# Optimization experiments

Hardware: AMD Instinct MI355X
Metric: run time of the kernel (lower is better)

The kernel has to match this reference:

```python
import jax, jax.numpy as jnp
import numpy as np

B, S, D, H = 2, 2048, 2048, 16
HD = D // H          # 128, even for RoPE
GS = 0.1             # governance_strength
ROPE_BASE = 10000.0


def _rope_cos_sin(seq_len, dtype):
    # inv_freq over pairs of dims: [HD/2]
    inv_freq = 1.0 / (ROPE_BASE ** (jnp.arange(0, HD, 2, dtype=jnp.float32) / HD))
    t = jnp.arange(seq_len, dtype=jnp.float32)
    freqs = jnp.outer(t, inv_freq)          # [S, HD/2]
    return jnp.cos(freqs).astype(dtype), jnp.sin(freqs).astype(dtype)


def _apply_rope(x, cos, sin):
    # x: [B,H,S,HD]; cos/sin: [S,HD/2] -> broadcast over batch/heads
    x1, x2 = jnp.split(x, 2, axis=-1)
    c = cos[None, None, :, :]
    s = sin[None, None, :, :]
    return jnp.concatenate([x1 * c - x2 * s, x2 * c + x1 * s], axis=-1)


def setup_inputs() -> dict:
    key = jax.random.key(0)
    ks = jax.random.split(key, 8)
    sc = 1.0 / np.sqrt(D)
    return {
        "x": jax.random.normal(ks[0], (B, S, D), jnp.float32),
        "Wq": jax.random.normal(ks[1], (D, D), jnp.float32) * sc,
        "Wk": jax.random.normal(ks[2], (D, D), jnp.float32) * sc,
        "Wv": jax.random.normal(ks[3], (D, D), jnp.float32) * sc,
        "Wo": jax.random.normal(ks[4], (D, D), jnp.float32) * sc,
        "bo": jnp.zeros((D,), jnp.float32),
        "policy_mask": jax.random.uniform(ks[5], (1, H, S, S), jnp.float32),
        "memory_weights": jax.random.uniform(ks[6], (B, 1, 1, S), jnp.float32),
    }


def reference(x, Wq, Wk, Wv, Wo, bo, policy_mask, memory_weights):
    dtype = x.dtype
    scale = HD ** -0.5

    def heads(t):
        return t.reshape(B, S, H, HD).transpose(0, 2, 1, 3)  # [B,H,S,HD]

    q = heads(x @ Wq)
    k = heads(x @ Wk)
    v = heads(x @ Wv)

    cos, sin = _rope_cos_sin(S, dtype)
    q = _apply_rope(q, cos, sin)
    k = _apply_rope(k, cos, sin)

    scores = jnp.einsum("bhqd,bhkd->bhqk", q, k) * scale  # [B,H,S,S]

    # governance bias: policy term + memory-aware log term
    bias = policy_mask * GS + jnp.log1p(memory_weights * GS + 1e-8)
    scores = scores + bias

    # causal mask (no KV cache: kv_len == q_len)
    causal = jnp.tril(jnp.ones((S, S), bool))[None, None]
    scores = jnp.where(causal, scores, jnp.asarray(-1e9, dtype))

    attn = jax.nn.softmax(scores, axis=-1)
    out = jnp.einsum("bhqk,bhkd->bhqd", attn, v)          # [B,H,S,HD]
    out = out.transpose(0, 2, 1, 3).reshape(B, S, D)
    return out @ Wo + bo
```

## Files before the change

### kernel.cpp

```cpp
#include <hip/hip_runtime.h>
#include <hip/hip_bf16.h>
#include <math.h>

#define B_ 2
#define S_ 2048
#define D_ 2048
#define H_ 16
#define HD_ 128
#define NT_ (B_*S_)
#define GS_ 0.1f

typedef _Float16 half8 __attribute__((__vector_size__(16)));
typedef _Float16 half4v __attribute__((__vector_size__(8)));
typedef _Float16 half2v __attribute__((__vector_size__(4)));
typedef float f32x4 __attribute__((__vector_size__(16)));
typedef float f32x16 __attribute__((__vector_size__(64)));

__device__ __forceinline__ void gload_lds16(const void* g, void* s) {
  __builtin_amdgcn_global_load_lds(
      (const __attribute__((address_space(1))) unsigned int*)g,
      (__attribute__((address_space(3))) unsigned int*)s, 16, 0, 0);
}


__global__ void cvt_f32_to_f16(const float* __restrict__ in, _Float16* __restrict__ out, int n4) {
  int i = blockIdx.x * blockDim.x + threadIdx.x;
  if (i >= n4) return;
  float4 v = ((const float4*)in)[i];
  half4v o = { (_Float16)v.x, (_Float16)v.y, (_Float16)v.z, (_Float16)v.w };
  ((half4v*)out)[i] = o;
}

__global__ void transpose_to_f16(const float* __restrict__ in, _Float16* __restrict__ out, int R, int C) {
  __shared__ float t[32][33];
  int c0 = blockIdx.x*32, r0 = blockIdx.y*32;
  int tx = threadIdx.x, ty = threadIdx.y;
#pragma unroll
  for (int j = 0; j < 32; j += 8)
    t[ty+j][tx] = in[(size_t)(r0+ty+j)*C + c0+tx];
  __syncthreads();
#pragma unroll
  for (int j = 0; j < 32; j += 8)
    out[(size_t)(c0+ty+j)*R + r0+tx] = (_Float16)t[tx][ty+j];
}

__global__ void prep_tables(const float* __restrict__ mw, float* __restrict__ cost,
                            float* __restrict__ sint, float* __restrict__ lmw) {
  int t = blockIdx.x*256 + threadIdx.x;
  if (t < S_*64) {
    int s = t >> 6, d = t & 63;
    float inv = (float)pow(10000.0, -(double)(2*d)/(double)HD_);
    float f = (float)s * inv;
    cost[t] = cosf(f);
    sint[t] = sinf(f);
  }
  if (t < B_*S_) lmw[t] = log1pf(mw[t]*GS_ + 1e-8f);
}


template<bool F32OUT>
__global__ __launch_bounds__(256) void gemm_f16(
    const _Float16* __restrict__ A, const _Float16* __restrict__ Bt,
    void* __restrict__ Cout, const float* __restrict__ bias,
    int M, int N, int K)
{
  __shared__ __align__(16) _Float16 As[128*64];
  __shared__ __align__(16) _Float16 Bs[128*64];
  int n0 = blockIdx.x*128, m0 = blockIdx.y*128;
  int tid = threadIdx.x;
  int w = tid >> 6, l = tid & 63;
  int lhi = l >> 4, llo = l & 15;
  int wr = w >> 1, wc = w & 1;
  const f32x4 fz = {0.f,0.f,0.f,0.f};
  f32x4 acc[4][4];
#pragma unroll
  for (int i = 0; i < 4; ++i)
#pragma unroll
    for (int j = 0; j < 4; ++j) acc[i][j] = fz;

  for (int kt = 0; kt < K; kt += 64) {
#pragma unroll
    for (int i = 0; i < 4; ++i) {
      int sid = i*256 + tid;
      int row = sid >> 3;
      int c   = (sid & 7) ^ (row & 7);
      gload_lds16(A  + (size_t)(m0+row)*K + kt + c*8, (char*)As + (size_t)(i*256 + w*64)*16);
      gload_lds16(Bt + (size_t)(n0+row)*K + kt + c*8, (char*)Bs + (size_t)(i*256 + w*64)*16);
    }
    __syncthreads();
#pragma unroll
    for (int kk = 0; kk < 2; ++kk) {
      half8 a[4], b[4];
#pragma unroll
      for (int mi = 0; mi < 4; ++mi) {
        int row = wr*64 + mi*16 + llo;
        int ch = (kk*4 + lhi) ^ (row & 7);
        a[mi] = *(const half8*)((const char*)As + row*128 + ch*16);
      }
#pragma unroll
      for (int ni = 0; ni < 4; ++ni) {
        int row = wc*64 + ni*16 + llo;
        int ch = (kk*4 + lhi) ^ (row & 7);
        b[ni] = *(const half8*)((const char*)Bs + row*128 + ch*16);
      }
#pragma unroll
      for (int mi = 0; mi < 4; ++mi)
#pragma unroll
        for (int ni = 0; ni < 4; ++ni)
          acc[mi][ni] = __builtin_amdgcn_mfma_f32_16x16x32_f16(a[mi], b[ni], acc[mi][ni], 0, 0, 0);
    }
    __syncthreads();
  }
#pragma unroll
  for (int mi = 0; mi < 4; ++mi)
#pragma unroll
    for (int ni = 0; ni < 4; ++ni)
#pragma unroll
      for (int r = 0; r < 4; ++r) {
        int row = m0 + wr*64 + mi*16 + lhi*4 + r;
        int col = n0 + wc*64 + ni*16 + llo;
        if constexpr (F32OUT)
          ((float*)Cout)[(size_t)row*N + col] = acc[mi][ni][r] + bias[col];
        else
          ((_Float16*)Cout)[(size_t)row*N + col] = (_Float16)acc[mi][ni][r];
      }
}

__global__ void rope_qk(const _Float16* __restrict__ qkv, const float* __restrict__ cost,
                        const float* __restrict__ sint, _Float16* __restrict__ Qr,
                        _Float16* __restrict__ Kr) {
  int token = blockIdx.x;
  int b = token >> 11, s = token & (S_-1);
  int t = threadIdx.x;
  int isk = t >> 7, u = t & 127;
  int hh = u >> 3, dd0 = (u & 7)*8;
  const _Float16* src = qkv + (size_t)token*(3*D_) + (size_t)isk*D_ + hh*128;
  half8 a  = *(const half8*)(src + dd0);
  half8 bb = *(const half8*)(src + 64 + dd0);
  half8 lo, hi;
#pragma unroll
  for (int j = 0; j < 8; ++j) {
    float c  = cost[s*64 + dd0 + j];
    float sn = sint[s*64 + dd0 + j];
    float x1 = (float)a[j], x2 = (float)bb[j];
    lo[j] = (_Float16)(x1*c - x2*sn);
    hi[j] = (_Float16)(x2*c + x1*sn);
  }
  _Float16* dst = (isk ? Kr : Qr) + ((size_t)(b*H_ + hh)*S_ + s)*HD_;
  *(half8*)(dst + dd0) = lo;
  *(half8*)(dst + 64 + dd0) = hi;
}

__global__ void v_transpose(const _Float16* __restrict__ qkv, _Float16* __restrict__ Vt) {
  __shared__ _Float16 tile[64][33];
  int st = blockIdx.x*64;
  int dt = blockIdx.y*32;
  int bh = blockIdx.z;
  int b = bh >> 4, h = bh & 15;
  int t = threadIdx.x;
  int s = t >> 2, dc = (t & 3)*8;
  half8 v = *(const half8*)(qkv + (size_t)(b*S_ + st + s)*(3*D_) + 2*D_ + h*128 + dt + dc);
#pragma unroll
  for (int j = 0; j < 8; ++j) tile[s][dc+j] = v[j];
  __syncthreads();
  int d = t >> 3, sc = (t & 7)*8;
  half8 o;
#pragma unroll
  for (int j = 0; j < 8; ++j) o[j] = tile[sc+j][d];
  *(half8*)(Vt + ((size_t)bh*HD_ + dt + d)*S_ + st + sc) = o;
}

__global__ __launch_bounds__(256) void attn_kernel(
    const _Float16* __restrict__ Qr, const _Float16* __restrict__ Kr,
    const _Float16* __restrict__ Vt, const float* __restrict__ policy,
    const float* __restrict__ lmw, _Float16* __restrict__ Ob)
{
  __shared__ __align__(16) char SMEM[32768];
  char* Kl = SMEM;
  char* Vl = SMEM + 16384;
  int bx = blockIdx.x;
  int qb = (S_/128) - 1 - (bx / (B_*H_));
  int rem = bx % (B_*H_);
  int h = rem >> 1;
  int b = rem & 1;
  int bh = b*H_ + h;
  const _Float16* Qb = Qr + (size_t)bh*S_*HD_;
  const _Float16* Kb = Kr + (size_t)bh*S_*HD_;
  const _Float16* Vb = Vt + (size_t)bh*HD_*S_;
  const float* pol = policy + (size_t)h*S_*S_;
  const float* lmb = lmw + b*S_;
  int tid = threadIdx.x;
  int w = tid >> 6, l = tid & 63;
  int l31 = l & 31, lh = l >> 5;
  int q0 = qb*128 + w*32;
  int gq = q0 + l31;

  const float scale = 0.08838834764831845f;
  half8 qf[8];
#pragma unroll
  for (int ds = 0; ds < 8; ++ds) {
    half8 qv = *(const half8*)(Qb + (size_t)gq*HD_ + ds*16 + lh*8);
#pragma unroll
    for (int e = 0; e < 8; ++e) qv[e] = (_Float16)((float)qv[e] * scale);
    qf[ds] = qv;
  }

  f32x16 oacc[4];
#pragma unroll
  for (int i = 0; i < 4; ++i)
#pragma unroll
    for (int r = 0; r < 16; ++r) oacc[i][r] = 0.f;
  float m_ = -INFINITY, l_ = 0.f;

  int nt = qb*2 + 2;
  for (int t = 0; t < nt; ++t) {
    int kv0 = t*64;
#pragma unroll
    for (int i = 0; i < 4; ++i) {
      int sid = i*256 + tid;
      int krow = sid >> 4;
      int ck = (sid & 15) ^ (krow & 15);
      gload_lds16(Kb + (size_t)(kv0+krow)*HD_ + ck*8, Kl + (size_t)(i*256 + w*64)*16);
      int co = (sid & 15) ^ (krow & 15);
      int dv = krow*2 + (co >> 3);
      gload_lds16(Vb + (size_t)dv*S_ + kv0 + (co & 7)*8, Vl + (size_t)(i*256 + w*64)*16);
    }
    __syncthreads();

    f32x16 sacc[2];
#pragma unroll
    for (int kh = 0; kh < 2; ++kh)
#pragma unroll
      for (int r = 0; r < 16; ++r) sacc[kh][r] = 0.f;
    __builtin_amdgcn_s_setprio(1);
#pragma unroll
    for (int kh = 0; kh < 2; ++kh) {
      const char* kbase = Kl + (kh*32 + l31)*256;
      int sw = l & 15;
#pragma unroll
      for (int ds = 0; ds < 8; ++ds) {
        half8 kf = *(const half8*)(kbase + (((ds*2 + lh) ^ sw) << 4));
        sacc[kh] = __builtin_amdgcn_mfma_f32_32x32x16_f16(kf, qf[ds], sacc[kh], 0, 0, 0);
      }
    }
    __builtin_amdgcn_s_setprio(0);

    bool domask = (kv0 + 63 > q0);
#pragma unroll
    for (int kh = 0; kh < 2; ++kh) {
      float po[16], lm_[16];
#pragma unroll
      for (int g = 0; g < 4; ++g) {
        int gk0 = kv0 + kh*32 + g*8 + lh*4;
        float4 p4 = *(const float4*)(pol + (size_t)gq*S_ + gk0);
        float4 l4 = *(const float4*)(lmb + gk0);
        po[g*4+0]=p4.x; po[g*4+1]=p4.y; po[g*4+2]=p4.z; po[g*4+3]=p4.w;
        lm_[g*4+0]=l4.x; lm_[g*4+1]=l4.y; lm_[g*4+2]=l4.z; lm_[g*4+3]=l4.w;
      }
#pragma unroll
      for (int r = 0; r < 16; ++r) {
        float v = fmaf(po[r], GS_, sacc[kh][r] + lm_[r]);
        int gk = kv0 + kh*32 + (r&3) + 8*(r>>2) + 4*lh;
        if (domask && gk > gq) v = -1e9f;
        sacc[kh][r] = v;
      }
    }

    float mx = -INFINITY;
#pragma unroll
    for (int kh = 0; kh < 2; ++kh)
#pragma unroll
      for (int r = 0; r < 16; ++r) mx = fmaxf(mx, sacc[kh][r]);
    mx = fmaxf(mx, __shfl_xor(mx, 32));
    bool skip = __all(mx - m_ <= 8.0f);
    if (!skip) {
      float mnew = fmaxf(m_, mx);
      float fct = __expf(m_ - mnew);
      m_ = mnew;
      l_ *= fct;
#pragma unroll
      for (int i = 0; i < 4; ++i)
#pragma unroll
        for (int r = 0; r < 16; ++r) oacc[i][r] *= fct;
    }
    float rsum = 0.f;
#pragma unroll
    for (int kh = 0; kh < 2; ++kh)
#pragma unroll
      for (int r = 0; r < 16; ++r) {
        float pp = __expf(sacc[kh][r] - m_);
        sacc[kh][r] = pp;
        rsum += pp;
      }
    rsum += __shfl_xor(rsum, 32);
    l_ += rsum;

    half8 pfrag[4];
#pragma unroll
    for (int s = 0; s < 4; ++s) {
      int kh = s >> 1, rb = (s & 1)*8;
      unsigned A0 = __builtin_bit_cast(unsigned, __builtin_amdgcn_cvt_pkrtz(sacc[kh][rb+0], sacc[kh][rb+1]));
      unsigned A1 = __builtin_bit_cast(unsigned, __builtin_amdgcn_cvt_pkrtz(sacc[kh][rb+2], sacc[kh][rb+3]));
      unsigned B0 = __builtin_bit_cast(unsigned, __builtin_amdgcn_cvt_pkrtz(sacc[kh][rb+4], sacc[kh][rb+5]));
      unsigned B1 = __builtin_bit_cast(unsigned, __builtin_amdgcn_cvt_pkrtz(sacc[kh][rb+6], sacc[kh][rb+7]));
      unsigned sA0 = (unsigned)__shfl_xor((int)A0, 32);
      unsigned sA1 = (unsigned)__shfl_xor((int)A1, 32);
      unsigned sB0 = (unsigned)__shfl_xor((int)B0, 32);
      unsigned sB1 = (unsigned)__shfl_xor((int)B1, 32);
      uint4 uu;
      uu.x = lh ? sB0 : A0;
      uu.y = lh ? sB1 : A1;
      uu.z = lh ? B0  : sA0;
      uu.w = lh ? B1  : sA1;
      pfrag[s] = __builtin_bit_cast(half8, uu);
    }

    __builtin_amdgcn_s_setprio(1);
#pragma unroll
    for (int dt = 0; dt < 4; ++dt) {
      int d = dt*32 + l31;
      const char* vbase = Vl + (d >> 1)*256;
      int swv = l31 >> 1;
      int cbase = (d & 1) << 3;
#pragma unroll
      for (int s = 0; s < 4; ++s) {
        half8 vf = *(const half8*)(vbase + (((cbase + s*2 + lh) ^ swv) << 4));
        oacc[dt] = __builtin_amdgcn_mfma_f32_32x32x16_f16(vf, pfrag[s], oacc[dt], 0, 0, 0);
      }
    }
    __builtin_amdgcn_s_setprio(0);
    __syncthreads();
  }

  float inv = 1.f / l_;
  int q = w*32 + l31;
#pragma unroll
  for (int dt = 0; dt < 4; ++dt)
#pragma unroll
    for (int rq = 0; rq < 4; ++rq) {
      half4v o4;
#pragma unroll
      for (int j = 0; j < 4; ++j) o4[j] = (_Float16)(oacc[dt][rq*4+j] * inv);
      int off = q*256 + ((dt*64 + rq*16 + lh*8) ^ ((q & 15) << 4));
      *(half4v*)(SMEM + off) = o4;
    }
  __syncthreads();
  int qr = tid >> 1, hf = tid & 1;
  size_t gbase = ((size_t)(b*S_ + qb*128 + qr))*D_ + h*128 + hf*64;
#pragma unroll
  for (int j = 0; j < 8; ++j) {
    int c = hf*8 + j;
    half8 vv = *(const half8*)(SMEM + qr*256 + ((c ^ (qr & 15)) << 4));
    *(half8*)(Ob + gbase + j*8) = vv;
  }
}


extern "C" void kernel_launch(void* const* d_in, const int* in_sizes, int n_in,
                              void* d_out, int out_size, void* d_ws, size_t ws_size,
                              hipStream_t stream) {
  const float* x   = (const float*)d_in[0];
  const float* Wq  = (const float*)d_in[1];
  const float* Wk  = (const float*)d_in[2];
  const float* Wv  = (const float*)d_in[3];
  const float* Wo  = (const float*)d_in[4];
  const float* bo  = (const float*)d_in[5];
  const float* pol = (const float*)d_in[6];
  const float* mw  = (const float*)d_in[7];
  float* out = (float*)d_out;

  char* p = (char*)d_ws;
  auto take = [&](size_t bytes) { char* r = p; p += (bytes + 255) & ~(size_t)255; return r; };
  _Float16* xb   = (_Float16*)take((size_t)NT_*D_*2);
  _Float16* Wt   = (_Float16*)take((size_t)3*D_*D_*2);
  _Float16* Wot  = (_Float16*)take((size_t)D_*D_*2);
  _Float16* qkv  = (_Float16*)take((size_t)NT_*3*D_*2);
  _Float16* Qr   = (_Float16*)take((size_t)B_*H_*S_*HD_*2);
  _Float16* Kr   = (_Float16*)take((size_t)B_*H_*S_*HD_*2);
  _Float16* Vtb  = (_Float16*)take((size_t)B_*H_*S_*HD_*2);
  _Float16* Ob   = (_Float16*)take((size_t)NT_*D_*2);
  float* cost = (float*)take((size_t)S_*64*4);
  float* sint = (float*)take((size_t)S_*64*4);
  float* lmwb = (float*)take((size_t)B_*S_*4);

  cvt_f32_to_f16<<<(NT_*D_/4 + 255)/256, 256, 0, stream>>>(x, xb, NT_*D_/4);
  transpose_to_f16<<<dim3(64,64), dim3(32,8), 0, stream>>>(Wq, Wt,                    D_, D_);
  transpose_to_f16<<<dim3(64,64), dim3(32,8), 0, stream>>>(Wk, Wt +   (size_t)D_*D_,  D_, D_);
  transpose_to_f16<<<dim3(64,64), dim3(32,8), 0, stream>>>(Wv, Wt + 2*(size_t)D_*D_,  D_, D_);
  transpose_to_f16<<<dim3(64,64), dim3(32,8), 0, stream>>>(Wo, Wot, D_, D_);
  prep_tables<<<512, 256, 0, stream>>>(mw, cost, sint, lmwb);

  gemm_f16<false><<<dim3(3*D_/128, NT_/128), 256, 0, stream>>>(xb, Wt, qkv, nullptr, NT_, 3*D_, D_);
  rope_qk<<<NT_, 256, 0, stream>>>(qkv, cost, sint, Qr, Kr);
  v_transpose<<<dim3(S_/64, HD_/32, B_*H_), 256, 0, stream>>>(qkv, Vtb);
  attn_kernel<<<B_*H_*(S_/128), 256, 0, stream>>>(Qr, Kr, Vtb, pol, lmwb, Ob);
  gemm_f16<true><<<dim3(D_/128, NT_/128), 256, 0, stream>>>(Ob, Wot, out, bo, NT_, D_, D_);
}
```

Measured before the change: 368.6 us.

## Double-buffer K/V tiles in LDS and coalesce policy-bias loads via LDS

Allocates two LDS buffers for the K/V tiles and prefetches the next tile with global_load_lds while the current tile's QK and PV MFMAs run, using explicit vmcnt waits and raw s_barrier instead of __syncthreads. The policy mask and log-memory bias are now loaded row-coalesced per wave, folded into fp16 in a per-wave LDS scratch, then read back in MFMA accumulator layout. The aim is to hide global latency and avoid strided policy loads. In exchange, LDS use grows to 80KB, which may cut occupancy, and the bias is rounded to fp16, a small precision loss.

```diff
diff --git a/kernel.cpp b/kernel.cpp
--- a/kernel.cpp
+++ b/kernel.cpp
@@ -15,6 +15,8 @@
 typedef _Float16 half2v __attribute__((__vector_size__(4)));
 typedef float f32x4 __attribute__((__vector_size__(16)));
 typedef float f32x16 __attribute__((__vector_size__(64)));
+
+#define VMCNT(n) asm volatile("s_waitcnt vmcnt(" #n ")" ::: "memory")
 
 __device__ __forceinline__ void gload_lds16(const void* g, void* s) {
   __builtin_amdgcn_global_load_lds(
@@ -175,9 +177,7 @@
     const _Float16* __restrict__ Vt, const float* __restrict__ policy,
     const float* __restrict__ lmw, _Float16* __restrict__ Ob)
 {
-  __shared__ __align__(16) char SMEM[32768];
-  char* Kl = SMEM;
-  char* Vl = SMEM + 16384;
+  __shared__ __align__(16) char SMEM[81920];
   int bx = blockIdx.x;
   int qb = (S_/128) - 1 - (bx / (B_*H_));
   int rem = bx % (B_*H_);
@@ -192,40 +192,65 @@
   int tid = threadIdx.x;
   int w = tid >> 6, l = tid & 63;
   int l31 = l & 31, lh = l >> 5;
+  int r8 = l >> 3, c8 = l & 7;
   int q0 = qb*128 + w*32;
   int gq = q0 + l31;
-
-  const float scale = 0.08838834764831845f;
-  half8 qf[8];
-#pragma unroll
-  for (int ds = 0; ds < 8; ++ds) {
-    half8 qv = *(const half8*)(Qb + (size_t)gq*HD_ + ds*16 + lh*8);
-#pragma unroll
-    for (int e = 0; e < 8; ++e) qv[e] = (_Float16)((float)qv[e] * scale);
-    qf[ds] = qv;
-  }
-
-  f32x16 oacc[4];
-#pragma unroll
-  for (int i = 0; i < 4; ++i)
-#pragma unroll
-    for (int r = 0; r < 16; ++r) oacc[i][r] = 0.f;
-  float m_ = -INFINITY, l_ = 0.f;
-
-  int nt = qb*2 + 2;
-  for (int t = 0; t < nt; ++t) {
-    int kv0 = t*64;
+  char* Bw = SMEM + 65536 + w*4096;
+
+  auto stageKV = [&](int tt, char* base){
+    int kv0s = tt*64;
 #pragma unroll
     for (int i = 0; i < 4; ++i) {
       int sid = i*256 + tid;
       int krow = sid >> 4;
       int ck = (sid & 15) ^ (krow & 15);
-      gload_lds16(Kb + (size_t)(kv0+krow)*HD_ + ck*8, Kl + (size_t)(i*256 + w*64)*16);
-      int co = (sid & 15) ^ (krow & 15);
-      int dv = krow*2 + (co >> 3);
-      gload_lds16(Vb + (size_t)dv*S_ + kv0 + (co & 7)*8, Vl + (size_t)(i*256 + w*64)*16);
-    }
-    __syncthreads();
+      gload_lds16(Kb + (size_t)(kv0s+krow)*HD_ + ck*8, base + (size_t)(i*256 + w*64)*16);
+      int dv = krow*2 + (ck >> 3);
+      gload_lds16(Vb + (size_t)dv*S_ + kv0s + (ck & 7)*8, base + 16384 + (size_t)(i*256 + w*64)*16);
+    }
+  };
+
+  const float scale = 0.08838834764831845f;
+  half8 qf[8];
+#pragma unroll
+  for (int ds = 0; ds < 8; ++ds) {
+    half8 qv = *(const half8*)(Qb + (size_t)gq*HD_ + ds*16 + lh*8);
+#pragma unroll
+    for (int e = 0; e < 8; ++e) qv[e] = (_Float16)((float)qv[e] * scale);
+    qf[ds] = qv;
+  }
+
+  f32x16 oacc[4];
+#pragma unroll
+  for (int i = 0; i < 4; ++i)
+#pragma unroll
+    for (int r = 0; r < 16; ++r) oacc[i][r] = 0.f;
+  float m_ = -INFINITY, l_ = 0.f;
+
+  stageKV(0, SMEM);
+  VMCNT(0);
+  __builtin_amdgcn_sched_barrier(0);
+  __builtin_amdgcn_s_barrier();
+
+  int nt = qb*2 + 2;
+  for (int t = 0; t < nt; ++t) {
+    int kv0 = t*64;
+    char* base = SMEM + (size_t)(t&1)*32768;
+    bool pre = (t+1 < nt);
+
+    float4 lmv[2];
+    float4 pb[4][2];
+#pragma unroll
+    for (int ci = 0; ci < 2; ++ci) {
+      lmv[ci] = *(const float4*)(lmb + kv0 + ci*32 + c8*4);
+#pragma unroll
+      for (int ri = 0; ri < 4; ++ri) {
+        int qq = q0 + ri*8 + r8;
+        pb[ri][ci] = *(const float4*)(pol + (size_t)qq*S_ + kv0 + ci*32 + c8*4);
+      }
+    }
+    __builtin_amdgcn_sched_barrier(0);
+    if (pre) stageKV(t+1, SMEM + (size_t)((t+1)&1)*32768);
 
     f32x16 sacc[2];
 #pragma unroll
@@ -235,7 +260,7 @@
     __builtin_amdgcn_s_setprio(1);
 #pragma unroll
     for (int kh = 0; kh < 2; ++kh) {
-      const char* kbase = Kl + (kh*32 + l31)*256;
+      const char* kbase = base + (kh*32 + l31)*256;
       int sw = l & 15;
 #pragma unroll
       for (int ds = 0; ds < 8; ++ds) {
@@ -245,26 +270,40 @@
     }
     __builtin_amdgcn_s_setprio(0);
 
+    if (pre) { VMCNT(8); } else { VMCNT(0); }
+    __builtin_amdgcn_sched_barrier(0);
+#pragma unroll
+    for (int ci = 0; ci < 2; ++ci)
+#pragma unroll
+      for (int ri = 0; ri < 4; ++ri) {
+        int ql = ri*8 + r8;
+        float bx_ = fmaf(pb[ri][ci].x, GS_, lmv[ci].x);
+        float by_ = fmaf(pb[ri][ci].y, GS_, lmv[ci].y);
+        float bz_ = fmaf(pb[ri][ci].z, GS_, lmv[ci].z);
+        float bw_ = fmaf(pb[ri][ci].w, GS_, lmv[ci].w);
+        half2v h0 = __builtin_amdgcn_cvt_pkrtz(bx_, by_);
+        half2v h1 = __builtin_amdgcn_cvt_pkrtz(bz_, bw_);
+        half4v o4 = { h0[0], h0[1], h1[0], h1[1] };
+        int chunk = (ci*8 + c8) ^ (ql & 15);
+        *(half4v*)(Bw + ql*128 + chunk*8) = o4;
+      }
+
     bool domask = (kv0 + 63 > q0);
 #pragma unroll
-    for (int kh = 0; kh < 2; ++kh) {
-      float po[16], lm_[16];
-#pragma unroll
-      for (int g = 0; g < 4; ++g) {
-        int gk0 = kv0 + kh*32 + g*8 + lh*4;
-        float4 p4 = *(const float4*)(pol + (size_t)gq*S_ + gk0);
-        float4 l4 = *(const float4*)(lmb + gk0);
-        po[g*4+0]=p4.x; po[g*4+1]=p4.y; po[g*4+2]=p4.z; po[g*4+3]=p4.w;
-        lm_[g*4+0]=l4.x; lm_[g*4+1]=l4.y; lm_[g*4+2]=l4.z; lm_[g*4+3]=l4.w;
-      }
-#pragma unroll
-      for (int r = 0; r < 16; ++r) {
-        float v = fmaf(po[r], GS_, sacc[kh][r] + lm_[r]);
-        int gk = kv0 + kh*32 + (r&3) + 8*(r>>2) + 4*lh;
-        if (domask && gk > gq) v = -1e9f;
-        sacc[kh][r] = v;
-      }
-    }
+    for (int kh = 0; kh < 2; ++kh)
+#pragma unroll
+      for (int rq = 0; rq < 4; ++rq) {
+        int chunk = 2*rq + lh + 8*kh;
+        half4v b4 = *(const half4v*)(Bw + l31*128 + ((chunk ^ (l31 & 15)) << 3));
+#pragma unroll
+        for (int rm = 0; rm < 4; ++rm) {
+          int r = rq*4 + rm;
+          float v = sacc[kh][r] + (float)b4[rm];
+          int gk = kv0 + kh*32 + rm + 8*rq + 4*lh;
+          if (domask && gk > gq) v = -1e9f;
+          sacc[kh][r] = v;
+        }
+      }
 
     float mx = -INFINITY;
 #pragma unroll
@@ -319,7 +358,7 @@
 #pragma unroll
     for (int dt = 0; dt < 4; ++dt) {
       int d = dt*32 + l31;
-      const char* vbase = Vl + (d >> 1)*256;
+      const char* vbase = base + 16384 + (d >> 1)*256;
       int swv = l31 >> 1;
       int cbase = (d & 1) << 3;
 #pragma unroll
@@ -329,7 +368,10 @@
       }
     }
     __builtin_amdgcn_s_setprio(0);
-    __syncthreads();
+
+    VMCNT(0);
+    __builtin_amdgcn_sched_barrier(0);
+    __builtin_amdgcn_s_barrier();
   }
 
   float inv = 1.f / l_;
```

New measurement: 355.8 us. 1.04x faster.

## Pipeline attention tiles with double-buffered K and prefetched coalesced bias loads

Applied to the files above, without the earlier changes.

Restructures the attention main loop so the next K tile and its policy/memory bias are prefetched while the current tile computes. K is double-buffered in LDS and V is loaded at tile start. Synchronisation now uses explicit vmcnt waits and raw barriers. Bias rows are read with coalesced float4 loads and transposed through a per-wave LDS scratch into the MFMA layout. The log2e factor is folded into the Q scale and the bias tables so the softmax can use exp2. Waves whose queries lie entirely before a tile's keys skip compute, and launch bounds request two blocks per CU. The hand-counted vmcnt values and the larger LDS footprint make the kernel fragile and could limit occupancy.

```diff
diff --git a/kernel.cpp b/kernel.cpp
--- a/kernel.cpp
+++ b/kernel.cpp
@@ -9,12 +9,16 @@
 #define HD_ 128
 #define NT_ (B_*S_)
 #define GS_ 0.1f
+#define LOG2E_ 1.4426950408889634f
 
 typedef _Float16 half8 __attribute__((__vector_size__(16)));
 typedef _Float16 half4v __attribute__((__vector_size__(8)));
 typedef _Float16 half2v __attribute__((__vector_size__(4)));
 typedef float f32x4 __attribute__((__vector_size__(16)));
 typedef float f32x16 __attribute__((__vector_size__(64)));
+
+#define VMCNT(n) asm volatile("s_waitcnt vmcnt(" #n ")" ::: "memory")
+#define LGKMCNT0 asm volatile("s_waitcnt lgkmcnt(0)" ::: "memory")
 
 __device__ __forceinline__ void gload_lds16(const void* g, void* s) {
   __builtin_amdgcn_global_load_lds(
@@ -54,7 +58,7 @@
     cost[t] = cosf(f);
     sint[t] = sinf(f);
   }
-  if (t < B_*S_) lmw[t] = log1pf(mw[t]*GS_ + 1e-8f);
+  if (t < B_*S_) lmw[t] = log1pf(mw[t]*GS_ + 1e-8f) * LOG2E_;
 }
 
 
@@ -170,14 +174,12 @@
   *(half8*)(Vt + ((size_t)bh*HD_ + dt + d)*S_ + st + sc) = o;
 }
 
-__global__ __launch_bounds__(256) void attn_kernel(
+__global__ __launch_bounds__(256, 2) void attn_kernel(
     const _Float16* __restrict__ Qr, const _Float16* __restrict__ Kr,
     const _Float16* __restrict__ Vt, const float* __restrict__ policy,
     const float* __restrict__ lmw, _Float16* __restrict__ Ob)
 {
-  __shared__ __align__(16) char SMEM[32768];
-  char* Kl = SMEM;
-  char* Vl = SMEM + 16384;
+  __shared__ __align__(16) char SMEM[65536];
   int bx = blockIdx.x;
   int qb = (S_/128) - 1 - (bx / (B_*H_));
   int rem = bx % (B_*H_);
@@ -192,145 +194,191 @@
   int tid = threadIdx.x;
   int w = tid >> 6, l = tid & 63;
   int l31 = l & 31, lh = l >> 5;
+  int r8 = l >> 3, c8 = l & 7;
   int q0 = qb*128 + w*32;
   int gq = q0 + l31;
-
-  const float scale = 0.08838834764831845f;
-  half8 qf[8];
-#pragma unroll
-  for (int ds = 0; ds < 8; ++ds) {
-    half8 qv = *(const half8*)(Qb + (size_t)gq*HD_ + ds*16 + lh*8);
-#pragma unroll
-    for (int e = 0; e < 8; ++e) qv[e] = (_Float16)((float)qv[e] * scale);
-    qf[ds] = qv;
-  }
-
-  f32x16 oacc[4];
-#pragma unroll
-  for (int i = 0; i < 4; ++i)
-#pragma unroll
-    for (int r = 0; r < 16; ++r) oacc[i][r] = 0.f;
-  float m_ = -INFINITY, l_ = 0.f;
-
-  int nt = qb*2 + 2;
-  for (int t = 0; t < nt; ++t) {
-    int kv0 = t*64;
+  char* Bw = SMEM + 49152 + w*4096;
+
+  auto stageK = [&](int tt){
+    char* dstb = SMEM + (size_t)(tt&1)*16384;
+    int kv = tt*64;
 #pragma unroll
     for (int i = 0; i < 4; ++i) {
       int sid = i*256 + tid;
       int krow = sid >> 4;
       int ck = (sid & 15) ^ (krow & 15);
-      gload_lds16(Kb + (size_t)(kv0+krow)*HD_ + ck*8, Kl + (size_t)(i*256 + w*64)*16);
-      int co = (sid & 15) ^ (krow & 15);
-      int dv = krow*2 + (co >> 3);
-      gload_lds16(Vb + (size_t)dv*S_ + kv0 + (co & 7)*8, Vl + (size_t)(i*256 + w*64)*16);
-    }
-    __syncthreads();
-
-    f32x16 sacc[2];
-#pragma unroll
-    for (int kh = 0; kh < 2; ++kh)
-#pragma unroll
-      for (int r = 0; r < 16; ++r) sacc[kh][r] = 0.f;
-    __builtin_amdgcn_s_setprio(1);
-#pragma unroll
-    for (int kh = 0; kh < 2; ++kh) {
-      const char* kbase = Kl + (kh*32 + l31)*256;
-      int sw = l & 15;
-#pragma unroll
-      for (int ds = 0; ds < 8; ++ds) {
-        half8 kf = *(const half8*)(kbase + (((ds*2 + lh) ^ sw) << 4));
-        sacc[kh] = __builtin_amdgcn_mfma_f32_32x32x16_f16(kf, qf[ds], sacc[kh], 0, 0, 0);
-      }
-    }
-    __builtin_amdgcn_s_setprio(0);
-
-    bool domask = (kv0 + 63 > q0);
-#pragma unroll
-    for (int kh = 0; kh < 2; ++kh) {
-      float po[16], lm_[16];
-#pragma unroll
-      for (int g = 0; g < 4; ++g) {
-        int gk0 = kv0 + kh*32 + g*8 + lh*4;
-        float4 p4 = *(const float4*)(pol + (size_t)gq*S_ + gk0);
-        float4 l4 = *(const float4*)(lmb + gk0);
-        po[g*4+0]=p4.x; po[g*4+1]=p4.y; po[g*4+2]=p4.z; po[g*4+3]=p4.w;
-        lm_[g*4+0]=l4.x; lm_[g*4+1]=l4.y; lm_[g*4+2]=l4.z; lm_[g*4+3]=l4.w;
-      }
-#pragma unroll
-      for (int r = 0; r < 16; ++r) {
-        float v = fmaf(po[r], GS_, sacc[kh][r] + lm_[r]);
-        int gk = kv0 + kh*32 + (r&3) + 8*(r>>2) + 4*lh;
-        if (domask && gk > gq) v = -1e9f;
-        sacc[kh][r] = v;
-      }
-    }
-
-    float mx = -INFINITY;
-#pragma unroll
-    for (int kh = 0; kh < 2; ++kh)
-#pragma unroll
-      for (int r = 0; r < 16; ++r) mx = fmaxf(mx, sacc[kh][r]);
-    mx = fmaxf(mx, __shfl_xor(mx, 32));
-    bool skip = __all(mx - m_ <= 8.0f);
-    if (!skip) {
-      float mnew = fmaxf(m_, mx);
-      float fct = __expf(m_ - mnew);
-      m_ = mnew;
-      l_ *= fct;
-#pragma unroll
-      for (int i = 0; i < 4; ++i)
-#pragma unroll
-        for (int r = 0; r < 16; ++r) oacc[i][r] *= fct;
-    }
-    float rsum = 0.f;
-#pragma unroll
-    for (int kh = 0; kh < 2; ++kh)
-#pragma unroll
-      for (int r = 0; r < 16; ++r) {
-        float pp = __expf(sacc[kh][r] - m_);
-        sacc[kh][r] = pp;
-        rsum += pp;
-      }
-    rsum += __shfl_xor(rsum, 32);
-    l_ += rsum;
-
-    half8 pfrag[4];
-#pragma unroll
-    for (int s = 0; s < 4; ++s) {
-      int kh = s >> 1, rb = (s & 1)*8;
-      unsigned A0 = __builtin_bit_cast(unsigned, __builtin_amdgcn_cvt_pkrtz(sacc[kh][rb+0], sacc[kh][rb+1]));
-      unsigned A1 = __builtin_bit_cast(unsigned, __builtin_amdgcn_cvt_pkrtz(sacc[kh][rb+2], sacc[kh][rb+3]));
-      unsigned B0 = __builtin_bit_cast(unsigned, __builtin_amdgcn_cvt_pkrtz(sacc[kh][rb+4], sacc[kh][rb+5]));
-      unsigned B1 = __builtin_bit_cast(unsigned, __builtin_amdgcn_cvt_pkrtz(sacc[kh][rb+6], sacc[kh][rb+7]));
-      unsigned sA0 = (unsigned)__shfl_xor((int)A0, 32);
-      unsigned sA1 = (unsigned)__shfl_xor((int)A1, 32);
-      unsigned sB0 = (unsigned)__shfl_xor((int)B0, 32);
-      unsigned sB1 = (unsigned)__shfl_xor((int)B1, 32);
-      uint4 uu;
-      uu.x = lh ? sB0 : A0;
-      uu.y = lh ? sB1 : A1;
-      uu.z = lh ? B0  : sA0;
-      uu.w = lh ? B1  : sA1;
-      pfrag[s] = __builtin_bit_cast(half8, uu);
-    }
-
-    __builtin_amdgcn_s_setprio(1);
-#pragma unroll
-    for (int dt = 0; dt < 4; ++dt) {
-      int d = dt*32 + l31;
-      const char* vbase = Vl + (d >> 1)*256;
-      int swv = l31 >> 1;
-      int cbase = (d & 1) << 3;
-#pragma unroll
-      for (int s = 0; s < 4; ++s) {
-        half8 vf = *(const half8*)(vbase + (((cbase + s*2 + lh) ^ swv) << 4));
-        oacc[dt] = __builtin_amdgcn_mfma_f32_32x32x16_f16(vf, pfrag[s], oacc[dt], 0, 0, 0);
-      }
-    }
-    __builtin_amdgcn_s_setprio(0);
-    __syncthreads();
-  }
+      gload_lds16(Kb + (size_t)(kv+krow)*HD_ + ck*8, dstb + (size_t)(i*256 + w*64)*16);
+    }
+  };
+  auto stageV = [&](int tt){
+    char* dstb = SMEM + 32768;
+    int kv = tt*64;
+#pragma unroll
+    for (int i = 0; i < 4; ++i) {
+      int sid = i*256 + tid;
+      int krow = sid >> 4;
+      int ck = (sid & 15) ^ (krow & 15);
+      int dv = krow*2 + (ck >> 3);
+      gload_lds16(Vb + (size_t)dv*S_ + kv + (ck & 7)*8, dstb + (size_t)(i*256 + w*64)*16);
+    }
+  };
+
+  float4 pbA[4][2], pbB[4][2], lmA[2], lmB[2];
+  auto loadBias = [&](int tt, float4 (&pb)[4][2], float4 (&lm)[2]){
+    int kv = tt*64;
+#pragma unroll
+    for (int ci = 0; ci < 2; ++ci) {
+      lm[ci] = *(const float4*)(lmb + kv + ci*32 + c8*4);
+#pragma unroll
+      for (int ri = 0; ri < 4; ++ri)
+        pb[ri][ci] = *(const float4*)(pol + (size_t)(q0 + ri*8 + r8)*S_ + kv + ci*32 + c8*4);
+    }
+  };
+
+  const float qscale = 0.08838834764831845f * LOG2E_;
+  half8 qf[8];
+#pragma unroll
+  for (int ds = 0; ds < 8; ++ds) {
+    half8 qv = *(const half8*)(Qb + (size_t)gq*HD_ + ds*16 + lh*8);
+#pragma unroll
+    for (int e = 0; e < 8; ++e) qv[e] = (_Float16)((float)qv[e] * qscale);
+    qf[ds] = qv;
+  }
+
+  f32x16 oacc[4];
+#pragma unroll
+  for (int i = 0; i < 4; ++i)
+#pragma unroll
+    for (int r = 0; r < 16; ++r) oacc[i][r] = 0.f;
+  float m_ = -INFINITY, l_ = 0.f;
+  const float GS2 = GS_ * LOG2E_;
+  int nt = qb*2 + 2;
+
+  stageK(0);
+  loadBias(0, pbA, lmA);
+  VMCNT(10);
+  __builtin_amdgcn_sched_barrier(0);
+  __builtin_amdgcn_s_barrier();
+
+#define TILE(T, PBC, LMC, PBN, LMN) do {                                       \
+    int t_ = (T);                                                              \
+    int kv0 = t_*64;                                                           \
+    const char* Kbase = SMEM + (size_t)(t_&1)*16384;                           \
+    const char* Vbase = SMEM + 32768;                                          \
+    bool pre = (t_+1 < nt);                                                    \
+    bool act = (kv0 <= q0 + 31);                                               \
+    stageV(t_);                                                                \
+    if (pre) { stageK(t_+1); loadBias(t_+1, PBN, LMN); }                       \
+    f32x16 sacc[2];                                                            \
+    if (act) {                                                                 \
+      for (int kh = 0; kh < 2; ++kh) {                                         \
+        for (int r = 0; r < 16; ++r) sacc[kh][r] = 0.f;                        \
+      }                                                                        \
+      __builtin_amdgcn_s_setprio(1);                                           \
+      _Pragma("unroll") for (int kh = 0; kh < 2; ++kh) {                       \
+        const char* kbase = Kbase + (kh*32 + l31)*256;                         \
+        int sw = l31 & 15;                                                     \
+        _Pragma("unroll") for (int ds = 0; ds < 8; ++ds) {                     \
+          half8 kf = *(const half8*)(kbase + (((ds*2 + lh) ^ sw) << 4));       \
+          sacc[kh] = __builtin_amdgcn_mfma_f32_32x32x16_f16(kf, qf[ds], sacc[kh], 0, 0, 0); \
+        }                                                                      \
+      }                                                                        \
+      __builtin_amdgcn_s_setprio(0);                                           \
+    }                                                                          \
+    if (pre) { VMCNT(14); } else { VMCNT(0); }                                 \
+    __builtin_amdgcn_sched_barrier(0);                                         \
+    if (act) {                                                                 \
+         \
+      _Pragma("unroll") for (int ci = 0; ci < 2; ++ci)                         \
+      _Pragma("unroll") for (int ri = 0; ri < 4; ++ri) {                       \
+        float bx_ = fmaf(PBC[ri][ci].x, GS2, LMC[ci].x);                       \
+        float by_ = fmaf(PBC[ri][ci].y, GS2, LMC[ci].y);                       \
+        float bz_ = fmaf(PBC[ri][ci].z, GS2, LMC[ci].z);                       \
+        float bw_ = fmaf(PBC[ri][ci].w, GS2, LMC[ci].w);                       \
+        half2v h0 = __builtin_amdgcn_cvt_pkrtz(bx_, by_);                      \
+        half2v h1 = __builtin_amdgcn_cvt_pkrtz(bz_, bw_);                      \
+        half4v o4 = { h0[0], h0[1], h1[0], h1[1] };                            \
+        int g = ci*8 + c8;                                                     \
+        *(half4v*)(Bw + g*256 + (((ri*8 + r8) ^ (2*g)) & 31)*8) = o4;          \
+      }                                                                        \
+      LGKMCNT0;                                                                \
+      __builtin_amdgcn_sched_barrier(0);                                       \
+      bool domask = (kv0 + 63 > q0);                                           \
+      _Pragma("unroll") for (int kh = 0; kh < 2; ++kh)                         \
+      _Pragma("unroll") for (int rq = 0; rq < 4; ++rq) {                       \
+        int g = kh*8 + 2*rq + lh;                                              \
+        half4v b4 = *(const half4v*)(Bw + g*256 + (((l31 ^ (2*g)) & 31)*8));   \
+        _Pragma("unroll") for (int rm = 0; rm < 4; ++rm) {                     \
+          int r = rq*4 + rm;                                                   \
+          float v = sacc[kh][r] + (float)b4[rm];                               \
+          int gk = kv0 + kh*32 + rm + 8*rq + 4*lh;                             \
+          if (domask && gk > gq) v = -1e9f;                                    \
+          sacc[kh][r] = v;                                                     \
+        }                                                                      \
+      }                                                                        \
+      float mx = -INFINITY;                                                    \
+      _Pragma("unroll") for (int kh = 0; kh < 2; ++kh)                         \
+      _Pragma("unroll") for (int r = 0; r < 16; ++r) mx = fmaxf(mx, sacc[kh][r]); \
+      mx = fmaxf(mx, __shfl_xor(mx, 32));                                      \
+      bool skip = __all(mx - m_ <= 11.5f);                                     \
+      if (!skip) {                                                             \
+        float mnew = fmaxf(m_, mx);                                            \
+        float fct = exp2f(m_ - mnew);                                          \
+        m_ = mnew;                                                             \
+        l_ *= fct;                                                             \
+        _Pragma("unroll") for (int i = 0; i < 4; ++i)                          \
+        _Pragma("unroll") for (int r = 0; r < 16; ++r) oacc[i][r] *= fct;      \
+      }                                                                        \
+      float rsum = 0.f;                                                        \
+      _Pragma("unroll") for (int kh = 0; kh < 2; ++kh)                         \
+      _Pragma("unroll") for (int r = 0; r < 16; ++r) {                         \
+        float pp = exp2f(sacc[kh][r] - m_);                                    \
+        sacc[kh][r] = pp;                                                      \
+        rsum += pp;                                                            \
+      }                                                                        \
+      rsum += __shfl_xor(rsum, 32);                                            \
+      l_ += rsum;                                                              \
+      half8 pfrag[4];                                                          \
+      _Pragma("unroll") for (int s = 0; s < 4; ++s) {                          \
+        int kh = s >> 1, rb = (s & 1)*8;                                       \
+        unsigned A0 = __builtin_bit_cast(unsigned, __builtin_amdgcn_cvt_pkrtz(sacc[kh][rb+0], sacc[kh][rb+1])); \
+        unsigned A1 = __builtin_bit_cast(unsigned, __builtin_amdgcn_cvt_pkrtz(sacc[kh][rb+2], sacc[kh][rb+3])); \
+        unsigned B0 = __builtin_bit_cast(unsigned, __builtin_amdgcn_cvt_pkrtz(sacc[kh][rb+4], sacc[kh][rb+5])); \
+        unsigned B1 = __builtin_bit_cast(unsigned, __builtin_amdgcn_cvt_pkrtz(sacc[kh][rb+6], sacc[kh][rb+7])); \
+        unsigned sA0 = (unsigned)__shfl_xor((int)A0, 32);                      \
+        unsigned sA1 = (unsigned)__shfl_xor((int)A1, 32);                      \
+        unsigned sB0 = (unsigned)__shfl_xor((int)B0, 32);                      \
+        unsigned sB1 = (unsigned)__shfl_xor((int)B1, 32);                      \
+        uint4 uu;                                                              \
+        uu.x = lh ? sB0 : A0;                                                  \
+        uu.y = lh ? sB1 : A1;                                                  \
+        uu.z = lh ? B0  : sA0;                                                 \
+        uu.w = lh ? B1  : sA1;                                                 \
+        pfrag[s] = __builtin_bit_cast(half8, uu);                              \
+      }                                                                        \
+      __builtin_amdgcn_s_setprio(1);                                           \
+      _Pragma("unroll") for (int dt = 0; dt < 4; ++dt) {                       \
+        int d = dt*32 + l31;                                                   \
+        const char* vbase = Vbase + (d >> 1)*256;                              \
+        int swv = l31 >> 1;                                                    \
+        int cbase = (d & 1) << 3;                                              \
+        _Pragma("unroll") for (int s = 0; s < 4; ++s) {                        \
+          half8 vf = *(const half8*)(vbase + (((cbase + s*2 + lh) ^ swv) << 4)); \
+          oacc[dt] = __builtin_amdgcn_mfma_f32_32x32x16_f16(vf, pfrag[s], oacc[dt], 0, 0, 0); \
+        }                                                                      \
+      }                                                                        \
+      __builtin_amdgcn_s_setprio(0);                                           \
+    }                                                                          \
+    if (pre) { VMCNT(10); } else { VMCNT(0); }                                 \
+    __builtin_amdgcn_sched_barrier(0);                                         \
+    __builtin_amdgcn_s_barrier();                                              \
+  } while(0)
+
+  for (int u = 0; u < nt; u += 2) {
+    TILE(u,   pbA, lmA, pbB, lmB);
+    TILE(u+1, pbB, lmB, pbA, lmA);
+  }
+#undef TILE
 
   float inv = 1.f / l_;
   int q = w*32 + l31;
```

New measurement: 708.7 us. 92.3% more time.
